# Performance work log

Hardware: AMD Instinct MI355X
Metric: run time of the kernel (lower is better)

The kernel has to match this reference:

```python
import jax, jax.numpy as jnp
import numpy as np

B, Q, P, HID = 1, 1024, 1024, 4096
NH, NKV, D = 32, 4, 128
MAXPOS = 2048
N_REP = NH // NKV


def rotate_half(x):
    x1, x2 = jnp.split(x, 2, axis=-1)
    return jnp.concatenate((-x2, x1), axis=-1)


def setup_inputs() -> dict:
    key = jax.random.key(0)
    ks = jax.random.split(key, 8)
    hidden_states = jax.random.normal(ks[0], (B, Q, HID), jnp.float32) * 0.02
    past_key_value = jax.random.normal(ks[1], (B, 2, NKV, P, D), jnp.float32)
    # additive causal mask buffer covering [B, NH, MAXPOS, MAXPOS]
    tril = jnp.tril(jnp.ones((MAXPOS, MAXPOS), jnp.bool_))
    mask2d = jnp.where(tril, 0.0, -1e9).astype(jnp.float32)
    attention_mask = jnp.broadcast_to(mask2d[None, None], (B, NH, MAXPOS, MAXPOS))
    Wq = jax.random.normal(ks[2], (HID, HID), jnp.float32) * 0.02
    Wk = jax.random.normal(ks[3], (NKV * D, HID), jnp.float32) * 0.02
    Wv = jax.random.normal(ks[4], (NKV * D, HID), jnp.float32) * 0.02
    Wo = jax.random.normal(ks[5], (HID, HID), jnp.float32) * 0.02
    return {"hidden_states": hidden_states, "past_key_value": past_key_value,
            "attention_mask": attention_mask, "Wq": Wq, "Wk": Wk, "Wv": Wv, "Wo": Wo}


def reference(hidden_states, past_key_value, attention_mask, Wq, Wk, Wv, Wo):
    kv_len = P + Q
    # projections (torch Linear: y = x @ W^T)
    q = jnp.einsum('bqh,oh->bqo', hidden_states, Wq).reshape(B, Q, NH, D).transpose(0, 2, 1, 3)
    k = jnp.einsum('bqh,oh->bqo', hidden_states, Wk).reshape(B, Q, NKV, D).transpose(0, 2, 1, 3)
    v = jnp.einsum('bqh,oh->bqo', hidden_states, Wv).reshape(B, Q, NKV, D).transpose(0, 2, 1, 3)
    # append to KV cache BEFORE RoPE (faithful to source ordering)
    past_k = past_key_value[:, 0]  # [B, NKV, P, D]
    past_v = past_key_value[:, 1]
    k = jnp.concatenate((past_k, k), axis=2)  # [B, NKV, kv_len, D]
    v = jnp.concatenate((past_v, v), axis=2)
    new_past = jnp.stack((k, v), axis=1)
    # rotary embedding: keys use positions [0, kv_len), queries [P, kv_len)
    inv_freq = 1.0 / (10000.0 ** (jnp.arange(0, D, 2, dtype=jnp.float32) / D))
    t = jnp.arange(kv_len, dtype=jnp.float32)
    freqs = jnp.einsum('i,j->ij', t, inv_freq)
    emb = jnp.concatenate((freqs, freqs), axis=-1)  # [kv_len, D]
    cos = jnp.cos(emb)[None, None]  # [1,1,kv_len,D]
    sin = jnp.sin(emb)[None, None]
    q = q * cos[:, :, P:kv_len] + rotate_half(q) * sin[:, :, P:kv_len]
    k = k * cos + rotate_half(k) * sin
    # causal mask slice: rows [kv_len-Q, kv_len), cols [0, kv_len)
    causal_mask = attention_mask[:, :, P:kv_len, :kv_len]
    # GQA broadcast of KV heads
    k = jnp.repeat(k, N_REP, axis=1)  # [B, NH, kv_len, D]
    v = jnp.repeat(v, N_REP, axis=1)
    scores = jnp.einsum('bhqd,bhkd->bhqk', q, k) / np.sqrt(D).astype(np.float32)
    scores = scores + causal_mask
    probs = jax.nn.softmax(scores, axis=-1)
    ctx = jnp.einsum('bhqk,bhkd->bhqd', probs, v)  # [B, NH, Q, D]
    ctx = ctx.transpose(0, 2, 1, 3).reshape(B, Q, HID)
    attn_output = jnp.einsum('bqh,oh->bqo', ctx, Wo)
    return attn_output, new_past
```

## Files before the change

### kernel.cpp

```cpp
#include <hip/hip_runtime.h>
#include <cstdint>
#include <cstddef>

typedef __attribute__((ext_vector_type(4))) float f32x4;
typedef __attribute__((ext_vector_type(8))) unsigned short u16x8;
typedef __attribute__((ext_vector_type(4))) unsigned short u16x4;
typedef __bf16 bf16x8 __attribute__((ext_vector_type(8)));

__device__ __forceinline__ unsigned short f2bf(float f) {
  unsigned u = __builtin_bit_cast(unsigned, f);
  u += 0x7FFF + ((u >> 16) & 1);
  return (unsigned short)(u >> 16);
}

__device__ __forceinline__ void mfma16x16x32(f32x4& acc, u16x8 a, u16x8 b) {
  acc = __builtin_amdgcn_mfma_f32_16x16x32_bf16(
      __builtin_bit_cast(bf16x8, a), __builtin_bit_cast(bf16x8, b), acc, 0, 0, 0);
}

typedef __attribute__((address_space(1))) const unsigned int as1_u32;
typedef __attribute__((address_space(3))) unsigned int as3_u32;
__device__ __forceinline__ void load_lds16(const void* g, void* l) {
  __builtin_amdgcn_global_load_lds((as1_u32*)g, (as3_u32*)l, 16, 0, 0);
}

#define QSCALE2 0.12751745f

__global__ void k_cvt_all(const float* __restrict__ hs, const float* __restrict__ wq,
                          const float* __restrict__ wk, const float* __restrict__ wv,
                          const float* __restrict__ wo,
                          unsigned short* __restrict__ hs_bf, unsigned short* __restrict__ w_bf,
                          float2* __restrict__ tab) {
  const int total = 10616832;
  int stride = gridDim.x * blockDim.x;
  for (int i = blockIdx.x * blockDim.x + threadIdx.x; i < total; i += stride) {
    if (i >= 10485760) {
      int j = i - 10485760;
      int t = j >> 6, f = j & 63;
      float inv = expf(-(float)f * 0.14391156831212787f);
      float ang = (float)t * inv;
      tab[j] = make_float2(cosf(ang), sinf(ang));
      continue;
    }
    const float4* src;
    unsigned short* dst;
    long j;
    if (i < 1048576) { src = (const float4*)hs; j = i; dst = hs_bf + (size_t)i * 4; }
    else {
      int t = i - 1048576;
      dst = w_bf + (size_t)t * 4;
      if (t < 4194304)      { src = (const float4*)wq; j = t; }
      else if (t < 4718592) { src = (const float4*)wk; j = t - 4194304; }
      else if (t < 5242880) { src = (const float4*)wv; j = t - 4718592; }
      else                  { src = (const float4*)wo; j = t - 5242880; }
    }
    float4 v = src[j];
    u16x4 o = { f2bf(v.x), f2bf(v.y), f2bf(v.z), f2bf(v.w) };
    *(u16x4*)dst = o;
  }
}

__global__ __launch_bounds__(256) void k_gemm_bt(
    const unsigned short* __restrict__ A, const unsigned short* __restrict__ Bt,
    float* __restrict__ C, int M, int N, int K, int KC) {
  __shared__ unsigned short lA[2][128 * 32];
  __shared__ unsigned short lB[2][128 * 32];
  const int tid = threadIdx.x;
  const int w = tid >> 6, lane = tid & 63;
  const int wm = w >> 1, wn = w & 1;
  const int m0 = blockIdx.y * 128, n0 = blockIdx.x * 128;
  const int k0 = blockIdx.z * KC;
  const int lr = lane & 15, lg = lane >> 4;
  float* Cp = C + (size_t)blockIdx.z * M * N;

  f32x4 acc[4][4];
#pragma unroll
  for (int i = 0; i < 4; i++)
#pragma unroll
    for (int j = 0; j < 4; j++) acc[i][j] = (f32x4){0.f, 0.f, 0.f, 0.f};

  const int srow = w * 32 + (lane >> 2);
  const int scol = (lane & 3) * 8;
  const unsigned short* gA = A + (size_t)(m0 + srow) * K + scol;
  const unsigned short* gB = Bt + (size_t)(n0 + srow) * K + scol;

  auto stage = [&](int buf, int kt) {
#pragma unroll
    for (int c = 0; c < 2; c++) {
      load_lds16(gA + (size_t)c * 16 * K + kt, &lA[buf][(w * 32 + c * 16) * 32]);
      load_lds16(gB + (size_t)c * 16 * K + kt, &lB[buf][(w * 32 + c * 16) * 32]);
    }
  };

  stage(0, k0);
  __syncthreads();
  int cur = 0;
  for (int kt = k0; kt < k0 + KC; kt += 32) {
    if (kt + 32 < k0 + KC) stage(cur ^ 1, kt + 32);
    u16x8 af[4], bf[4];
#pragma unroll
    for (int i = 0; i < 4; i++) af[i] = *(const u16x8*)&lA[cur][(wm * 64 + i * 16 + lr) * 32 + lg * 8];
#pragma unroll
    for (int j = 0; j < 4; j++) bf[j] = *(const u16x8*)&lB[cur][(wn * 64 + j * 16 + lr) * 32 + lg * 8];
#pragma unroll
    for (int i = 0; i < 4; i++)
#pragma unroll
      for (int j = 0; j < 4; j++) mfma16x16x32(acc[i][j], af[i], bf[j]);
    __syncthreads();
    cur ^= 1;
  }
#pragma unroll
  for (int i = 0; i < 4; i++)
#pragma unroll
    for (int j = 0; j < 4; j++)
#pragma unroll
      for (int r = 0; r < 4; r++) {
        int row = m0 + wm * 64 + i * 16 + lg * 4 + r;
        int col = n0 + wn * 64 + j * 16 + lr;
        Cp[(size_t)row * N + col] = acc[i][j][r];
      }
}

__global__ void k_reduce4(const float4* __restrict__ p, float4* __restrict__ out,
                          int n4, size_t stride4) {
  int stridet = gridDim.x * blockDim.x;
  for (int i = blockIdx.x * blockDim.x + threadIdx.x; i < n4; i += stridet) {
    float4 a = p[i], b = p[i + stride4], c = p[i + 2 * stride4], d = p[i + 3 * stride4];
    out[i] = make_float4((a.x + b.x) + (c.x + d.x), (a.y + b.y) + (c.y + d.y),
                         (a.z + b.z) + (c.z + d.z), (a.w + b.w) + (c.w + d.w));
  }
}

#define GP_S 5242880
__device__ __forceinline__ float gsum(const float* __restrict__ gp, size_t i) {
  return (gp[i] + gp[i + GP_S]) + (gp[i + 2 * (size_t)GP_S] + gp[i + 3 * (size_t)GP_S]);
}

__global__ void k_post(const float* __restrict__ past, const float* __restrict__ gp,
                       float* __restrict__ outk, float* __restrict__ outv,
                       unsigned short* __restrict__ kr, unsigned short* __restrict__ vt,
                       unsigned short* __restrict__ qr, const float2* __restrict__ tab) {
  int idx = blockIdx.x * blockDim.x + threadIdx.x;
  if (idx < 524288) {
    int d0 = idx & 63;
    int t = (idx >> 6) & 2047;
    int h = idx >> 17;
    float v1, v2;
    if (t < 1024) {
      const float* p = past + ((size_t)h * 1024 + t) * 128;
      v1 = p[d0]; v2 = p[d0 + 64];
    } else {
      size_t base = (size_t)(t - 1024) * 5120 + 4096 + h * 128;
      v1 = gsum(gp, base + d0); v2 = gsum(gp, base + d0 + 64);
    }
    float* o = outk + ((size_t)h * 2048 + t) * 128;
    o[d0] = v1; o[d0 + 64] = v2;
    float2 cs = tab[t * 64 + d0];
    unsigned short* ko = kr + ((size_t)h * 2048 + t) * 128;
    ko[d0]      = f2bf(v1 * cs.x - v2 * cs.y);
    ko[d0 + 64] = f2bf(v2 * cs.x + v1 * cs.y);
  } else if (idx < 1572864) {
    int i = idx - 524288;
    int d = i & 127;
    int t = (i >> 7) & 2047;
    int h = i >> 18;
    float val = (t < 1024) ? past[4 * 1024 * 128 + ((size_t)h * 1024 + t) * 128 + d]
                           : gsum(gp, (size_t)(t - 1024) * 5120 + 4608 + h * 128 + d);
    outv[((size_t)h * 2048 + t) * 128 + d] = val;
    vt[((size_t)h * 128 + d) * 2048 + t] = f2bf(val);
  } else {
    int i = idx - 1572864;
    int d0 = i & 63;
    int q = (i >> 6) & 1023;
    int h = i >> 16;
    size_t base = (size_t)q * 5120 + h * 128;
    float v1 = gsum(gp, base + d0), v2 = gsum(gp, base + d0 + 64);
    float2 cs = tab[(1024 + q) * 64 + d0];
    unsigned short* o = qr + ((size_t)h * 1024 + q) * 128;
    o[d0]      = f2bf((v1 * cs.x - v2 * cs.y) * QSCALE2);
    o[d0 + 64] = f2bf((v2 * cs.x + v1 * cs.y) * QSCALE2);
  }
}

__global__ __launch_bounds__(512) void k_attn8(
    const unsigned short* __restrict__ qr,
    const unsigned short* __restrict__ kr,
    const unsigned short* __restrict__ vt,
    unsigned short* __restrict__ ctxb) {
  __shared__ unsigned short k_lds[2][64 * 128];
  __shared__ unsigned short v_lds[2][128 * 64];
  __shared__ unsigned short plds[8][640];
  const int bid = blockIdx.x;
  const int h = bid >> 3;
  const int c = bid & 7;
  const int kvh = h >> 3;
  const int tid = threadIdx.x;
  const int w = tid >> 6, l = tid & 63;
  const int lr = l & 15, lg = l >> 4;
  const int q0 = c * 128 + w * 16;
  const unsigned short* kh = kr + (size_t)kvh * 2048 * 128;
  const unsigned short* vh = vt + (size_t)kvh * 128 * 2048;

  u16x8 qf[4];
  {
    const unsigned short* qb = qr + ((size_t)(h * 1024 + q0 + lr)) * 128 + lg * 8;
#pragma unroll
    for (int ks = 0; ks < 4; ks++) qf[ks] = *(const u16x8*)(qb + ks * 32);
  }
  f32x4 acc[8];
#pragma unroll
  for (int i = 0; i < 8; i++) acc[i] = (f32x4){0.f, 0.f, 0.f, 0.f};
  float m_r = -1e30f, l_r = 0.f;

  const int limit = 1024 + q0 + lr;
  const int mylimit = 1024 + q0 + 15;
  const int T = 18 + 2 * c;

  auto stageK = [&](int buf, int kb) {
#pragma unroll
    for (int i = 0; i < 2; i++) {
      int loff = i * 8192 + tid * 16;
      int row = loff >> 8;
      int scb = (loff & 255) ^ ((row & 7) << 4);
      load_lds16((const char*)(kh + (size_t)(kb + row) * 128) + scb,
                 (char*)&k_lds[buf][0] + loff);
    }
  };
  auto stageV = [&](int buf, int kb) {
#pragma unroll
    for (int i = 0; i < 2; i++) {
      int loff = i * 8192 + tid * 16;
      int row = loff >> 7;
      int scb = (loff & 127) ^ ((row & 7) << 4);
      load_lds16((const char*)(vh + (size_t)row * 2048 + kb) + scb,
                 (char*)&v_lds[buf][0] + loff);
    }
  };

  stageK(0, 0); stageV(0, 0);
  __syncthreads();
  int cur = 0;
  for (int t = 0; t < T; t++) {
    if (t + 1 < T) { stageK(cur ^ 1, (t + 1) * 64); stageV(cur ^ 1, (t + 1) * 64); }
    if (t * 64 <= mylimit) {
#pragma unroll
      for (int kc = 0; kc < 2; kc++) {
        const int kb = t * 64 + kc * 32;
        if (kb > mylimit) continue;
        f32x4 s[2];
#pragma unroll
        for (int sub = 0; sub < 2; sub++) {
          f32x4 a = (f32x4){0.f, 0.f, 0.f, 0.f};
          const int key = kc * 32 + sub * 16 + lr;
          const int swz = (key & 7) << 4;
#pragma unroll
          for (int ks = 0; ks < 4; ks++) {
            int addr = key * 256 + ((ks * 64 + lg * 16) ^ swz);
            u16x8 kf = *(const u16x8*)((const char*)&k_lds[cur][0] + addr);
            mfma16x16x32(a, kf, qf[ks]);
          }
          s[sub] = a;
        }
        float v[8];
#pragma unroll
        for (int r = 0; r < 4; r++) { v[r] = s[0][r]; v[4 + r] = s[1][r]; }
        if (kb + 31 > 1024 + q0) {
          const int kbase = kb + lg * 4;
#pragma unroll
          for (int r = 0; r < 4; r++) {
            if (kbase + r > limit)      v[r]     = -1e30f;
            if (kbase + 16 + r > limit) v[4 + r] = -1e30f;
          }
        }
        float tmax = v[0];
#pragma unroll
        for (int j = 1; j < 8; j++) tmax = fmaxf(tmax, v[j]);
        tmax = fmaxf(tmax, __shfl_xor(tmax, 16));
        tmax = fmaxf(tmax, __shfl_xor(tmax, 32));
        if (!__all(tmax <= m_r + 11.5f)) {
          float mn = fmaxf(m_r, tmax);
          float corr = exp2f(m_r - mn);
          m_r = mn;
          l_r *= corr;
#pragma unroll
          for (int nt = 0; nt < 8; nt++)
#pragma unroll
            for (int r = 0; r < 4; r++) acc[nt][r] *= corr;
        }
        float p[8];
        float psum = 0.f;
#pragma unroll
        for (int j = 0; j < 8; j++) { p[j] = exp2f(v[j] - m_r); psum += p[j]; }
        psum += __shfl_xor(psum, 16);
        psum += __shfl_xor(psum, 32);
        l_r += psum;
        unsigned wds[4];
#pragma unroll
        for (int j = 0; j < 4; j++) {
          unsigned lo = __builtin_bit_cast(unsigned, p[2 * j]) + 0x8000u;
          unsigned hi = __builtin_bit_cast(unsigned, p[2 * j + 1]) + 0x8000u;
          wds[j] = (hi & 0xFFFF0000u) | (lo >> 16);
        }
        char* pb = (char*)&plds[w][0] + lr * 80 + lg * 8;
        *(uint2*)(pb)      = make_uint2(wds[0], wds[1]);
        *(uint2*)(pb + 32) = make_uint2(wds[2], wds[3]);
        asm volatile("s_waitcnt lgkmcnt(0)" ::: "memory");
        u16x8 pf = *(const u16x8*)&plds[w][lr * 40 + lg * 8];
#pragma unroll
        for (int nt = 0; nt < 8; nt++) {
          const int d = nt * 16 + lr;
          int addr = d * 128 + ((kc * 64 + lg * 16) ^ ((d & 7) << 4));
          u16x8 vf = *(const u16x8*)((const char*)&v_lds[cur][0] + addr);
          mfma16x16x32(acc[nt], vf, pf);
        }
      }
    }
    __syncthreads();
    cur ^= 1;
  }
  float inv = 1.0f / l_r;
  unsigned short* ob = ctxb + (size_t)(q0 + lr) * 4096 + h * 128 + lg * 4;
#pragma unroll
  for (int nt = 0; nt < 8; nt++) {
    u16x4 o = { f2bf(acc[nt][0] * inv), f2bf(acc[nt][1] * inv),
                f2bf(acc[nt][2] * inv), f2bf(acc[nt][3] * inv) };
    *(u16x4*)(ob + nt * 16) = o;
  }
}

extern "C" void kernel_launch(void* const* d_in, const int* in_sizes, int n_in,
                              void* d_out, int out_size, void* d_ws, size_t ws_size,
                              hipStream_t stream) {
  (void)in_sizes; (void)n_in; (void)out_size; (void)ws_size;
  const float* hs   = (const float*)d_in[0];
  const float* past = (const float*)d_in[1];
  const float* Wq = (const float*)d_in[3];
  const float* Wk = (const float*)d_in[4];
  const float* Wv = (const float*)d_in[5];
  const float* Wo = (const float*)d_in[6];

  float* out_attn = (float*)d_out;
  float* out_pk = out_attn + 4194304;
  float* out_pv = out_pk + 1048576;

  const size_t MB = 1048576;
  char* ws = (char*)d_ws;
  unsigned short* hs_bf   = (unsigned short*)(ws);
  unsigned short* wqkv_bf = (unsigned short*)(ws + 8 * MB);
  unsigned short* wo_bf   = (unsigned short*)(ws + 48 * MB);
  float2*         tab     = (float2*)(ws + 100 * MB);
  unsigned short* kr      = (unsigned short*)(ws + 101 * MB);
  unsigned short* vt      = (unsigned short*)(ws + 103 * MB);
  unsigned short* qr      = (unsigned short*)(ws + 105 * MB);
  unsigned short* ctxb    = (unsigned short*)(ws + 113 * MB);
  float*          gp      = (float*)(ws + 128 * MB);

  k_cvt_all<<<2048, 256, 0, stream>>>(hs, Wq, Wk, Wv, Wo, hs_bf, wqkv_bf, tab);

  dim3 g1(5120 / 128, 1024 / 128, 4);
  k_gemm_bt<<<g1, 256, 0, stream>>>(hs_bf, wqkv_bf, gp, 1024, 5120, 4096, 1024);

  k_post<<<14336, 256, 0, stream>>>(past, gp, out_pk, out_pv, kr, vt, qr, tab);

  k_attn8<<<256, 512, 0, stream>>>(qr, kr, vt, ctxb);

  dim3 g2(4096 / 128, 1024 / 128, 4);
  k_gemm_bt<<<g2, 256, 0, stream>>>(ctxb, wo_bf, gp, 1024, 4096, 4096, 1024);
  k_reduce4<<<2048, 256, 0, stream>>>((const float4*)gp, (float4*)out_attn, 1048576, 1048576);
}
```

Measured before the change: 267.8 us.

## Fuse fp32 weight-to-bf16 conversion into GEMM B-tile staging and halve split-K

The separate pass that converts the weights to bf16 is removed. The GEMM now reads the fp32 Wq/Wk/Wv/Wo directly, converts them in registers and writes the bf16 tiles to LDS, with the B loads issued after the MFMAs so they overlap compute. Split-K drops from 4 to 2, with a matching change to the partial-sum reduction and the gsum in k_post, which cuts partial-buffer traffic. In exchange the B tile now needs twice the global read bytes per tile and synchronous register-path staging, and there are fewer blocks for parallelism.

```diff
diff --git a/kernel.cpp b/kernel.cpp
--- a/kernel.cpp
+++ b/kernel.cpp
@@ -26,42 +26,27 @@
 
 #define QSCALE2 0.12751745f
 
-__global__ void k_cvt_all(const float* __restrict__ hs, const float* __restrict__ wq,
-                          const float* __restrict__ wk, const float* __restrict__ wv,
-                          const float* __restrict__ wo,
-                          unsigned short* __restrict__ hs_bf, unsigned short* __restrict__ w_bf,
-                          float2* __restrict__ tab) {
-  const int total = 10616832;
-  int stride = gridDim.x * blockDim.x;
-  for (int i = blockIdx.x * blockDim.x + threadIdx.x; i < total; i += stride) {
-    if (i >= 10485760) {
-      int j = i - 10485760;
-      int t = j >> 6, f = j & 63;
-      float inv = expf(-(float)f * 0.14391156831212787f);
-      float ang = (float)t * inv;
-      tab[j] = make_float2(cosf(ang), sinf(ang));
-      continue;
-    }
-    const float4* src;
-    unsigned short* dst;
-    long j;
-    if (i < 1048576) { src = (const float4*)hs; j = i; dst = hs_bf + (size_t)i * 4; }
-    else {
-      int t = i - 1048576;
-      dst = w_bf + (size_t)t * 4;
-      if (t < 4194304)      { src = (const float4*)wq; j = t; }
-      else if (t < 4718592) { src = (const float4*)wk; j = t - 4194304; }
-      else if (t < 5242880) { src = (const float4*)wv; j = t - 4718592; }
-      else                  { src = (const float4*)wo; j = t - 5242880; }
-    }
-    float4 v = src[j];
+__global__ void k_cvt_small(const float* __restrict__ hs,
+                            unsigned short* __restrict__ hs_bf,
+                            float2* __restrict__ tab) {
+  int i = blockIdx.x * blockDim.x + threadIdx.x;
+  if (i < 1048576) {
+    float4 v = ((const float4*)hs)[i];
     u16x4 o = { f2bf(v.x), f2bf(v.y), f2bf(v.z), f2bf(v.w) };
-    *(u16x4*)dst = o;
-  }
-}
-
-__global__ __launch_bounds__(256) void k_gemm_bt(
-    const unsigned short* __restrict__ A, const unsigned short* __restrict__ Bt,
+    *(u16x4*)(hs_bf + (size_t)i * 4) = o;
+  } else {
+    int j = i - 1048576;
+    int t = j >> 6, f = j & 63;
+    float inv = expf(-(float)f * 0.14391156831212787f);
+    float ang = (float)t * inv;
+    tab[j] = make_float2(cosf(ang), sinf(ang));
+  }
+}
+
+__global__ __launch_bounds__(256, 3) void k_gemm_bf32(
+    const unsigned short* __restrict__ A,
+    const float* __restrict__ B1, const float* __restrict__ B2,
+    const float* __restrict__ B3, int nb1, int nb2,
     float* __restrict__ C, int M, int N, int K, int KC) {
   __shared__ unsigned short lA[2][128 * 32];
   __shared__ unsigned short lB[2][128 * 32];
@@ -73,6 +58,11 @@
   const int lr = lane & 15, lg = lane >> 4;
   float* Cp = C + (size_t)blockIdx.z * M * N;
 
+  const float* bp; int nn;
+  if (n0 < nb1)      { bp = B1; nn = n0; }
+  else if (n0 < nb2) { bp = B2; nn = n0 - nb1; }
+  else               { bp = B3; nn = n0 - nb2; }
+
   f32x4 acc[4][4];
 #pragma unroll
   for (int i = 0; i < 4; i++)
@@ -82,21 +72,34 @@
   const int srow = w * 32 + (lane >> 2);
   const int scol = (lane & 3) * 8;
   const unsigned short* gA = A + (size_t)(m0 + srow) * K + scol;
-  const unsigned short* gB = Bt + (size_t)(n0 + srow) * K + scol;
-
-  auto stage = [&](int buf, int kt) {
-#pragma unroll
-    for (int c = 0; c < 2; c++) {
+  const int br = tid >> 2, bseg = (tid & 3) * 8;
+  const float* gB0 = bp + (size_t)(nn + br) * K + bseg;
+  const float* gB1 = bp + (size_t)(nn + 64 + br) * K + bseg;
+
+  auto stageA = [&](int buf, int kt) {
+#pragma unroll
+    for (int c = 0; c < 2; c++)
       load_lds16(gA + (size_t)c * 16 * K + kt, &lA[buf][(w * 32 + c * 16) * 32]);
-      load_lds16(gB + (size_t)c * 16 * K + kt, &lB[buf][(w * 32 + c * 16) * 32]);
-    }
   };
-
-  stage(0, k0);
+  auto stageB = [&](int buf, int kt) {
+    float4 x0 = *(const float4*)(gB0 + kt);
+    float4 x1 = *(const float4*)(gB0 + kt + 4);
+    float4 y0 = *(const float4*)(gB1 + kt);
+    float4 y1 = *(const float4*)(gB1 + kt + 4);
+    u16x8 lo = { f2bf(x0.x), f2bf(x0.y), f2bf(x0.z), f2bf(x0.w),
+                 f2bf(x1.x), f2bf(x1.y), f2bf(x1.z), f2bf(x1.w) };
+    u16x8 hi = { f2bf(y0.x), f2bf(y0.y), f2bf(y0.z), f2bf(y0.w),
+                 f2bf(y1.x), f2bf(y1.y), f2bf(y1.z), f2bf(y1.w) };
+    *(u16x8*)&lB[buf][br * 32 + bseg] = lo;
+    *(u16x8*)&lB[buf][(64 + br) * 32 + bseg] = hi;
+  };
+
+  stageA(0, k0); stageB(0, k0);
   __syncthreads();
   int cur = 0;
   for (int kt = k0; kt < k0 + KC; kt += 32) {
-    if (kt + 32 < k0 + KC) stage(cur ^ 1, kt + 32);
+    const bool hasNext = (kt + 32 < k0 + KC);
+    if (hasNext) stageA(cur ^ 1, kt + 32);
     u16x8 af[4], bf[4];
 #pragma unroll
     for (int i = 0; i < 4; i++) af[i] = *(const u16x8*)&lA[cur][(wm * 64 + i * 16 + lr) * 32 + lg * 8];
@@ -106,6 +109,7 @@
     for (int i = 0; i < 4; i++)
 #pragma unroll
       for (int j = 0; j < 4; j++) mfma16x16x32(acc[i][j], af[i], bf[j]);
+    if (hasNext) stageB(cur ^ 1, kt + 32);
     __syncthreads();
     cur ^= 1;
   }
@@ -121,19 +125,18 @@
       }
 }
 
-__global__ void k_reduce4(const float4* __restrict__ p, float4* __restrict__ out,
-                          int n4, size_t stride4) {
+__global__ void k_reduce2(const float4* __restrict__ p, float4* __restrict__ out,
+                          int n4, size_t s4) {
   int stridet = gridDim.x * blockDim.x;
   for (int i = blockIdx.x * blockDim.x + threadIdx.x; i < n4; i += stridet) {
-    float4 a = p[i], b = p[i + stride4], c = p[i + 2 * stride4], d = p[i + 3 * stride4];
-    out[i] = make_float4((a.x + b.x) + (c.x + d.x), (a.y + b.y) + (c.y + d.y),
-                         (a.z + b.z) + (c.z + d.z), (a.w + b.w) + (c.w + d.w));
+    float4 a = p[i], b = p[i + s4];
+    out[i] = make_float4(a.x + b.x, a.y + b.y, a.z + b.z, a.w + b.w);
   }
 }
 
 #define GP_S 5242880
 __device__ __forceinline__ float gsum(const float* __restrict__ gp, size_t i) {
-  return (gp[i] + gp[i + GP_S]) + (gp[i + 2 * (size_t)GP_S] + gp[i + 3 * (size_t)GP_S]);
+  return gp[i] + gp[i + GP_S];
 }
 
 __global__ void k_post(const float* __restrict__ past, const float* __restrict__ gp,
@@ -346,8 +349,6 @@
   const size_t MB = 1048576;
   char* ws = (char*)d_ws;
   unsigned short* hs_bf   = (unsigned short*)(ws);
-  unsigned short* wqkv_bf = (unsigned short*)(ws + 8 * MB);
-  unsigned short* wo_bf   = (unsigned short*)(ws + 48 * MB);
   float2*         tab     = (float2*)(ws + 100 * MB);
   unsigned short* kr      = (unsigned short*)(ws + 101 * MB);
   unsigned short* vt      = (unsigned short*)(ws + 103 * MB);
@@ -355,16 +356,19 @@
   unsigned short* ctxb    = (unsigned short*)(ws + 113 * MB);
   float*          gp      = (float*)(ws + 128 * MB);
 
-  k_cvt_all<<<2048, 256, 0, stream>>>(hs, Wq, Wk, Wv, Wo, hs_bf, wqkv_bf, tab);
-
-  dim3 g1(5120 / 128, 1024 / 128, 4);
-  k_gemm_bt<<<g1, 256, 0, stream>>>(hs_bf, wqkv_bf, gp, 1024, 5120, 4096, 1024);
+  k_cvt_small<<<4608, 256, 0, stream>>>(hs, hs_bf, tab);
+
+  dim3 g1(5120 / 128, 1024 / 128, 2);
+  k_gemm_bf32<<<g1, 256, 0, stream>>>(hs_bf, Wq, Wk, Wv, 4096, 4608,
+                                      gp, 1024, 5120, 4096, 2048);
 
   k_post<<<14336, 256, 0, stream>>>(past, gp, out_pk, out_pv, kr, vt, qr, tab);
 
   k_attn8<<<256, 512, 0, stream>>>(qr, kr, vt, ctxb);
 
-  dim3 g2(4096 / 128, 1024 / 128, 4);
-  k_gemm_bt<<<g2, 256, 0, stream>>>(ctxb, wo_bf, gp, 1024, 4096, 4096, 1024);
-  k_reduce4<<<2048, 256, 0, stream>>>((const float4*)gp, (float4*)out_attn, 1048576, 1048576);
-}
+  dim3 g2(4096 / 128, 1024 / 128, 2);
+  k_gemm_bf32<<<g2, 256, 0, stream>>>(ctxb, Wo, Wo, Wo, 1 << 30, 1 << 30,
+                                      gp, 1024, 4096, 4096, 2048);
+  k_reduce2<<<2048, 256, 0, stream>>>((const float4*)gp, (float4*)out_attn,
+                                      1048576, 1048576);
+}
```

New measurement: 293.6 us. +9.6%, slower.
